# Performance work log

Hardware: AMD Instinct MI355X
Metric: run time of the kernel (lower is better)

## Reference

```python
import jax, jax.numpy as jnp
import numpy as np

# ---- static problem config (matches init_kwargs / input_specs) ----
L = 8                      # num_labels
D = H = W = 96             # volume dims
N = D * H * W
ALPHA, BETA, GAMMA = 8.0, 0.125, 3.0
NIT = 5                    # num_iterations
# 4-D bilateral grid dims: 3 spatial axes scaled by alpha, 1 intensity axis scaled by beta
GD = (int(np.ceil((D - 1) / ALPHA)) + 2,
      int(np.ceil((H - 1) / ALPHA)) + 2,
      int(np.ceil((W - 1) / ALPHA)) + 2,
      int(np.ceil(1.0 / BETA)) + 2)
GSIZE = int(np.prod(GD))
_STRIDES = np.array([GD[1] * GD[2] * GD[3], GD[2] * GD[3], GD[3], 1], dtype=np.int32)


def spatial_gaussian(Q):
    """Exact separable 3D Gaussian filter with sigma=GAMMA. Q: (L, D, H, W)."""
    r = int(3 * GAMMA)
    t = jnp.arange(-r, r + 1, dtype=Q.dtype)
    k = jnp.exp(-0.5 * (t / GAMMA) ** 2)
    k = k / k.sum()
    x = Q[None]  # (1, L, D, H, W)
    for ax in range(3):
        kspatial = [1, 1, 1]
        kspatial[ax] = 2 * r + 1
        kern = jnp.broadcast_to(k.reshape([1, 1] + kspatial), [L, 1] + kspatial)
        pad = [(r, r) if i == ax else (0, 0) for i in range(3)]
        x = jax.lax.conv_general_dilated(
            x, kern, (1, 1, 1), pad, feature_group_count=L,
            dimension_numbers=('NCDHW', 'OIDHW', 'NCDHW'))
    return x[0]


def splat_coords(img):
    """4-D lattice features per voxel. img: (D, H, W). Returns lo (4,N) int32, frac (4,N)."""
    zz, yy, xx = jnp.meshgrid(jnp.arange(D, dtype=img.dtype),
                              jnp.arange(H, dtype=img.dtype),
                              jnp.arange(W, dtype=img.dtype), indexing='ij')
    feats = jnp.stack([zz.reshape(-1) / ALPHA,
                       yy.reshape(-1) / ALPHA,
                       xx.reshape(-1) / ALPHA,
                       img.reshape(-1) / BETA], axis=0)  # (4, N)
    hi = jnp.asarray(GD, feats.dtype).reshape(4, 1) - 2.0
    lo_f = jnp.clip(jnp.floor(feats), 0.0, hi)
    frac = feats - lo_f
    return lo_f.astype(jnp.int32), frac


def blur1(g, ax):
    """[1,2,1]/4 blur along axis ax (grid-unit Gaussian of the splat-blur-slice)."""
    pad = [(0, 0)] * g.ndim
    pad[ax] = (1, 1)
    gp = jnp.pad(g, pad)
    n = g.shape[ax]
    a = jax.lax.slice_in_dim(gp, 0, n, axis=ax)
    b = jax.lax.slice_in_dim(gp, 1, n + 1, axis=ax)
    c = jax.lax.slice_in_dim(gp, 2, n + 2, axis=ax)
    return 0.25 * a + 0.5 * b + 0.25 * c


def lattice_filter(vals, lo, frac):
    """Splat-blur-slice high-dim Gaussian filter. vals: (C, N) -> (C, N)."""
    C = vals.shape[0]
    grid = jnp.zeros((C, GSIZE), vals.dtype)
    idxs, ws = [], []
    for bits in range(16):  # 16 corners of the 4-D cell (multilinear splat)
        off = np.array([(bits >> d) & 1 for d in range(4)], dtype=np.int32)
        w = jnp.prod(jnp.where(off[:, None] == 1, frac, 1.0 - frac), axis=0)  # (N,)
        idx = jnp.sum((lo + off[:, None]) * _STRIDES[:, None], axis=0)        # (N,)
        idxs.append(idx)
        ws.append(w)
        grid = grid.at[:, idx].add(vals * w[None])
    g = grid.reshape((C,) + GD)
    for ax in range(1, 5):
        g = blur1(g, ax)
    gf = g.reshape(C, GSIZE)
    out = jnp.zeros_like(vals)
    for bits in range(16):  # slice
        out = out + ws[bits][None] * gf[:, idxs[bits]]
    return out


def bilateral_apply(Q, lo, frac):
    """Normalized bilateral filtering of Q (L, D, H, W)."""
    vals = jnp.concatenate([Q.reshape(L, N), jnp.ones((1, N), Q.dtype)], axis=0)
    out = lattice_filter(vals, lo, frac)
    return (out[:L] / (out[L:] + 1e-8)).reshape(L, D, H, W)


def reference(U, image, spatial_ker_weights, bilateral_ker_weights, compatibility_matrix):
    Us = U[0]                               # (L, D, H, W); batch must be 1
    lo, frac = splat_coords(image[0, 0])    # lattice built once from image (as in __init__)
    Q = Us
    for _ in range(NIT):
        # NOTE: original code recomputes softmax of the (unchanged) unary U each iteration
        Qsm = jax.nn.softmax(Us, axis=0)
        sp = spatial_gaussian(Qsm).reshape(L, -1)
        bi = bilateral_apply(Qsm, lo, frac).reshape(L, -1)
        Qp = compatibility_matrix @ (spatial_ker_weights @ sp + bilateral_ker_weights @ bi)
        Q = Us + Qp.reshape(L, D, H, W)
    return jax.nn.softmax(Q, axis=0)[None]


def setup_inputs() -> dict:
    key = jax.random.key(0)
    k1, k2 = jax.random.split(key)
    U = jax.random.normal(k1, (1, L, D, H, W), jnp.float32)
    image = jax.random.uniform(k2, (1, 1, D, H, W), jnp.float32)
    eye = jnp.eye(L, dtype=jnp.float32)
    return {
        "U": U,
        "image": image,
        "spatial_ker_weights": 3.0 * eye,     # spatial_ker_weight * I
        "bilateral_ker_weights": 10.0 * eye,  # bilateral_ker_weight * I
        "compatibility_matrix": eye,
    }
```

## Files before the change

kernel.cpp:

```cpp
#include <hip/hip_runtime.h>
#include <math.h>

#define LBL   8
#define DIM   96
#define PLANE (DIM*DIM)
#define NVOX  (DIM*DIM*DIM)
#define GD0 14
#define GD1 14
#define GD2 14
#define GD3 10
#define GSIZE (GD0*GD1*GD2*GD3)
#define ST0 1960
#define ST1 140
#define ST2 10
#define CH  12
#define NBLK 12
#define NBLKS (NBLK*NBLK*NBLK)
#define PART 720
#define GOUT (GSIZE*9)
#define SUP 513
#define ROW8 (DIM/8)
#define PLANE8 (PLANE/8)
#define VOL8 (NVOX/8)

typedef _Float16 half8 __attribute__((ext_vector_type(8)));

__device__ inline half8 h8zero() {
    half8 v;
    #pragma unroll
    for (int e = 0; e < 8; ++e) v[e] = (_Float16)0.f;
    return v;
}

__constant__ float GW[10] = {
    0.13317604f, 0.12597912f, 0.10663904f, 0.08077540f, 0.05475300f,
    0.03320771f, 0.01802341f, 0.00875346f, 0.00380423f, 0.00147945f
};

__global__ __launch_bounds__(512)
void k_softmax_splat(const float* __restrict__ U, const float* __restrict__ img,
                     _Float16* __restrict__ q, float* __restrict__ part)
{
    __shared__ float sF[512];
    __shared__ __align__(16) unsigned char uball[2880 * 4];
    __shared__ _Float16 sA[64*180];

    _Float16* sU = (_Float16*)uball;
    float*    sB = (float*)uball;

    const int tid = threadIdx.x;
    const int bid0 = blockIdx.x;
    const int bid = (bid0 & 7) * (NBLKS >> 3) + (bid0 >> 3);
    const int bx = bid % NBLK;
    const int by = (bid / NBLK) % NBLK;
    const int bz = bid / (NBLK*NBLK);

    const int lx = tid & 7;
    const int ly = (tid >> 3) & 7;
    const int lz = tid >> 6;

    const int x = bx*8 + lx;
    const int y = by*8 + ly;
    const int z = bz*8 + lz;
    const int vox = z * PLANE + y * DIM + x;

    {
        float u[LBL];
        float m = -1e30f;
        #pragma unroll
        for (int l = 0; l < LBL; ++l) { u[l] = U[l*NVOX + vox]; m = fmaxf(m, u[l]); }
        float ssum = 0.f;
        #pragma unroll
        for (int l = 0; l < LBL; ++l) { u[l] = expf(u[l] - m); ssum += u[l]; }
        const float inv = 1.f / ssum;
        #pragma unroll
        for (int l = 0; l < LBL; ++l) {
            u[l] *= inv;
            q[l*NVOX + vox] = (_Float16)u[l];
            sU[l*SUP + tid] = (_Float16)u[l];
        }
        sU[8*SUP + tid] = (_Float16)1.0f;
        sF[tid] = img[vox] * 8.0f;
    }
    __syncthreads();

    {
        const int cgrp = tid & 3;
        const int k2   = (tid >> 2) & 1;
        const int row  = tid >> 3;
        const int cb   = cgrp * 2;

        float bins[10][3];
        #pragma unroll
        for (int g = 0; g < 10; ++g) { bins[g][0]=0.f; bins[g][1]=0.f; bins[g][2]=0.f; }

        for (int vx = 0; vx < 8; ++vx) {
            const int vi = row*8 + vx;
            const float f  = sF[vi];
            const float wx = k2 ? (float)vx*0.125f : 1.f - (float)vx*0.125f;
            const float u0 = (float)sU[cb*SUP + vi];
            const float u1 = (float)sU[(cb+1)*SUP + vi];
            const float u2 = (float)sU[8*SUP + vi];
            #pragma unroll
            for (int g = 0; g < 10; ++g) {
                float w = fmaxf(1.f - fabsf(f - (float)g), 0.f) * wx;
                bins[g][0] += w*u0; bins[g][1] += w*u1; bins[g][2] += w*u2;
            }
        }
        _Float16* pA = sA + row*180 + k2*90;
        #pragma unroll
        for (int g = 0; g < 10; ++g) {
            pA[g*9 + cb]     = (_Float16)bins[g][0];
            pA[g*9 + cb + 1] = (_Float16)bins[g][1];
            if (cgrp == 3) pA[g*9 + 8] = (_Float16)bins[g][2];
        }
    }
    __syncthreads();

    if (tid < 288) {
        const int c   = tid % 9;
        const int k2  = (tid / 9) & 1;
        const int j2  = (tid / 18) & 1;
        const int lzo = tid / 36;
        float S[10];
        #pragma unroll
        for (int g = 0; g < 10; ++g) S[g] = 0.f;
        for (int ly2 = 0; ly2 < 8; ++ly2) {
            const float wy = j2 ? (float)ly2*0.125f : 1.f - (float)ly2*0.125f;
            const _Float16* pA = sA + (lzo*8 + ly2)*180 + k2*90;
            #pragma unroll
            for (int g = 0; g < 10; ++g) S[g] += wy * (float)pA[g*9 + c];
        }
        float* pB = sB + lzo*360 + j2*180 + k2*90;
        #pragma unroll
        for (int g = 0; g < 10; ++g) pB[g*9 + c] = S[g];
    }
    __syncthreads();

    for (int item = tid; item < PART; item += 512) {
        const int t  = item / 90;
        const int gc = item % 90;
        const int i2 = t >> 2, j2 = (t >> 1) & 1, k2 = t & 1;
        float acc = 0.f;
        #pragma unroll
        for (int lzo = 0; lzo < 8; ++lzo) {
            const float wz = i2 ? (float)lzo*0.125f : 1.f - (float)lzo*0.125f;
            acc += wz * sB[lzo*360 + j2*180 + k2*90 + gc];
        }
        part[(size_t)bid*PART + item] = acc;
    }
}

__global__ __launch_bounds__(256)
void k_reduce(const float* __restrict__ part, float* __restrict__ grid)
{
    const int item = blockIdx.x*256 + threadIdx.x;
    if (item >= GOUT) return;
    const int c    = item % 9;
    const int cell = item / 9;
    const int gz = cell / ST0;
    int r = cell % ST0;
    const int gy = r / ST1;  r %= ST1;
    const int gx = r / ST2;
    const int g  = r % ST2;
    float acc = 0.f;
    #pragma unroll
    for (int t = 0; t < 8; ++t) {
        const int i2 = t >> 2, j2 = (t >> 1) & 1, k2 = t & 1;
        const int bz = gz - i2, by = gy - j2, bx = gx - k2;
        if ((unsigned)bz < (unsigned)NBLK && (unsigned)by < (unsigned)NBLK &&
            (unsigned)bx < (unsigned)NBLK)
            acc += part[(size_t)((bz*NBLK + by)*NBLK + bx)*PART + t*90 + g*9 + c];
    }
    grid[cell*CH + c] = acc;
}

__global__ __launch_bounds__(256)
void k_blur81(const float* __restrict__ src, float* __restrict__ dst)
{
    const int item = blockIdx.x*256 + threadIdx.x;
    if (item >= GOUT) return;
    const int c    = item % 9;
    const int cell = item / 9;
    const int gz = cell / ST0;
    int r = cell % ST0;
    const int gy = r / ST1;  r %= ST1;
    const int gx = r / ST2;
    const int g  = r % ST2;

    const int crd[4] = {gz, gy, gx, g};
    const int ext[4] = {GD0, GD1, GD2, GD3};
    const int str[4] = {ST0, ST1, ST2, 1};
    float wa[4][3];
    int   oa[4][3];
    #pragma unroll
    for (int ax = 0; ax < 4; ++ax)
        #pragma unroll
        for (int dd = 0; dd < 3; ++dd) {
            const int cc = crd[ax] + dd - 1;
            const bool ok = (cc >= 0 && cc < ext[ax]);
            wa[ax][dd] = ok ? (dd == 1 ? 0.5f : 0.25f) : 0.f;
            oa[ax][dd] = ok ? (dd - 1) * str[ax] : 0;
        }

    float acc = 0.f;
    #pragma unroll
    for (int a = 0; a < 3; ++a) {
        const float w0 = wa[0][a];
        #pragma unroll
        for (int b = 0; b < 3; ++b) {
            const float w1 = w0 * wa[1][b];
            #pragma unroll
            for (int d2 = 0; d2 < 3; ++d2) {
                const float w2 = w1 * wa[2][d2];
                const int ob = oa[0][a] + oa[1][b] + oa[2][d2];
                #pragma unroll
                for (int e = 0; e < 3; ++e)
                    acc += w2 * wa[3][e] * src[(cell + ob + oa[3][e])*CH + c];
            }
        }
    }
    dst[cell*CH + c] = acc;
}

__global__ __launch_bounds__(256)
void k_gauss_xy(const half8* __restrict__ src, half8* __restrict__ dst)
{
    __shared__ _Float16 sIn[PLANE];
    __shared__ _Float16 sX[PLANE];
    half8* sIn8 = (half8*)sIn;
    half8* sX8  = (half8*)sX;

    const int tid = threadIdx.x;
    const size_t base8 = (size_t)blockIdx.x * PLANE8;

    for (int i = tid; i < PLANE8; i += 256) sIn8[i] = src[base8 + i];
    __syncthreads();

    for (int it = tid; it < 576; it += 256) {
        const int seg = it % 6;
        const int row = it / 6;
        float w[48];
        #pragma unroll
        for (int k = 0; k < 6; ++k) {
            const int j8 = 2*seg - 2 + k;
            half8 v = h8zero();
            if (j8 >= 0 && j8 < ROW8) v = sIn8[row*ROW8 + j8];
            #pragma unroll
            for (int e = 0; e < 8; ++e) w[k*8 + e] = (float)v[e];
        }
        half8 o0 = h8zero(), o1 = h8zero();
        #pragma unroll
        for (int i = 0; i < 16; ++i) {
            float acc = 0.f;
            #pragma unroll
            for (int t = -9; t <= 9; ++t) acc += GW[t < 0 ? -t : t] * w[i + 16 + t];
            if (i < 8) o0[i] = (_Float16)acc; else o1[i - 8] = (_Float16)acc;
        }
        sX8[row*ROW8 + 2*seg]     = o0;
        sX8[row*ROW8 + 2*seg + 1] = o1;
    }
    __syncthreads();

    for (int it = tid; it < 288; it += 256) {
        const int x8   = it % ROW8;
        const int yseg = it / ROW8;
        const int ct = yseg * 4;
        float acc[4][8];
        #pragma unroll
        for (int k = 0; k < 4; ++k)
            #pragma unroll
            for (int e = 0; e < 8; ++e) acc[k][e] = 0.f;
        #pragma unroll
        for (int jj = 0; jj < 22; ++jj) {
            const int j = ct - 9 + jj;
            if (j < 0 || j >= DIM) continue;
            const half8 v = sX8[j*ROW8 + x8];
            float f[8];
            #pragma unroll
            for (int e = 0; e < 8; ++e) f[e] = (float)v[e];
            #pragma unroll
            for (int k = 0; k < 4; ++k) {
                const int d = jj - 9 - k;
                if (d >= -9 && d <= 9) {
                    const float wgt = GW[d < 0 ? -d : d];
                    #pragma unroll
                    for (int e = 0; e < 8; ++e) acc[k][e] += wgt * f[e];
                }
            }
        }
        #pragma unroll
        for (int k = 0; k < 4; ++k) {
            half8 o;
            #pragma unroll
            for (int e = 0; e < 8; ++e) o[e] = (_Float16)acc[k][e];
            dst[base8 + (ct + k)*ROW8 + x8] = o;
        }
    }
}

__global__ __launch_bounds__(256)
void k_gauss_z(const half8* __restrict__ src, half8* __restrict__ dst)
{
    const int bid = blockIdx.x;
    const int swz = (bid & 7) * (864 >> 3) + (bid >> 3);
    const int u = swz * 256 + threadIdx.x;

    const int x8 = u % ROW8;
    const int yy = (u / ROW8) % DIM;
    const int ztl = u / (ROW8 * DIM);
    const int zt = ztl % (DIM/4);
    const int l  = ztl / (DIM/4);
    const int base8 = l * VOL8 + yy * ROW8 + x8;
    const int ct = zt * 4;

    float acc[4][8];
    #pragma unroll
    for (int k = 0; k < 4; ++k)
        #pragma unroll
        for (int e = 0; e < 8; ++e) acc[k][e] = 0.f;

    #pragma unroll
    for (int jj = 0; jj < 22; ++jj) {
        const int j = ct - 9 + jj;
        if (j < 0 || j >= DIM) continue;
        const half8 v = src[base8 + j*PLANE8];
        float f[8];
        #pragma unroll
        for (int e = 0; e < 8; ++e) f[e] = (float)v[e];
        #pragma unroll
        for (int k = 0; k < 4; ++k) {
            const int d = jj - 9 - k;
            if (d >= -9 && d <= 9) {
                const float wgt = GW[d < 0 ? -d : d];
                #pragma unroll
                for (int e = 0; e < 8; ++e) acc[k][e] += wgt * f[e];
            }
        }
    }
    #pragma unroll
    for (int k = 0; k < 4; ++k) {
        half8 o;
        #pragma unroll
        for (int e = 0; e < 8; ++e) o[e] = (_Float16)acc[k][e];
        dst[base8 + (ct + k)*PLANE8] = o;
    }
}

__global__ __launch_bounds__(512)
void k_final(const float* __restrict__ U, const _Float16* __restrict__ sp,
             const float* __restrict__ grid, const float* __restrict__ img,
             const float* __restrict__ Cm, const float* __restrict__ Sw,
             const float* __restrict__ Bw, float* __restrict__ out)
{
    __shared__ float sm[128];
    __shared__ __align__(16) float sG[1800];

    const int tid = threadIdx.x;
    if (tid < 64) {
        const int i = tid >> 3, j = tid & 7;
        float cs = 0.f, cb = 0.f;
        #pragma unroll
        for (int k = 0; k < 8; ++k) {
            cs += Cm[i*8 + k] * Sw[k*8 + j];
            cb += Cm[i*8 + k] * Bw[k*8 + j];
        }
        sm[tid] = cs;
        sm[64 + tid] = cb;
    }

    const int bid0 = blockIdx.x;
    const int bid = (bid0 & 7) * (1728 >> 3) + (bid0 >> 3);
    const int bxi = bid % 3;
    const int byi = (bid / 3) % 6;
    const int z   = bid / 18;

    const int zc0 = z >> 3;
    const float fz = (float)(z & 7) * 0.125f;

    for (int item = tid; item < 1800; item += 512) {
        const int c    = item % 12;
        const int cell = item / 12;
        const int g  = cell % 10;
        const int xc = (cell / 10) % 5;
        const int yc = cell / 50;
        const int cellA = zc0*ST0 + (byi*2 + yc)*ST1 + (bxi*4 + xc)*ST2 + g;
        sG[item] = (1.f - fz)*grid[cellA*CH + c] + fz*grid[(cellA + ST0)*CH + c];
    }
    __syncthreads();

    const int lx  = tid & 31;
    const int lyt = tid >> 5;
    const int x = bxi*32 + lx;
    const int y = byi*16 + lyt;
    const int vox = z*PLANE + y*DIM + x;

    const float f = img[vox] * 8.0f;
    int li = (int)floorf(f);
    li = li < 0 ? 0 : (li > 8 ? 8 : li);
    const float fi = f - (float)li;
    const float fy = (float)(y & 7) * 0.125f;
    const float fx = (float)(x & 7) * 0.125f;
    const float wyv[2] = {1.f - fy, fy};
    const float wxv[2] = {1.f - fx, fx};
    const float wiv[2] = {1.f - fi, fi};
    const int ycb = lyt >> 3;
    const int xcb = lx >> 3;

    float acc[9];
    #pragma unroll
    for (int c = 0; c < 9; ++c) acc[c] = 0.f;

    #pragma unroll
    for (int j2 = 0; j2 < 2; ++j2)
    #pragma unroll
    for (int k2 = 0; k2 < 2; ++k2) {
        const float wsp = wyv[j2] * wxv[k2];
        const int base = (((ycb + j2)*5 + (xcb + k2))*10 + li)*12;
        #pragma unroll
        for (int m2 = 0; m2 < 2; ++m2) {
            const float w = wsp * wiv[m2];
            const float* p = &sG[base + m2*12];
            const float4 p0 = *reinterpret_cast<const float4*>(p);
            const float4 p1 = *reinterpret_cast<const float4*>(p + 4);
            acc[0] += w * p0.x; acc[1] += w * p0.y; acc[2] += w * p0.z; acc[3] += w * p0.w;
            acc[4] += w * p1.x; acc[5] += w * p1.y; acc[6] += w * p1.z; acc[7] += w * p1.w;
            acc[8] += w * p[8];
        }
    }
    const float dinv = 1.f / (acc[8] + 1e-8f);

    float spv[LBL], uu[LBL];
    #pragma unroll
    for (int l = 0; l < LBL; ++l) {
        spv[l] = (float)sp[(size_t)l*NVOX + vox];
        uu[l]  = U[(size_t)l*NVOX + vox];
    }

    float v[LBL];
    float mx = -1e30f;
    #pragma unroll
    for (int i = 0; i < LBL; ++i) {
        float t = 0.f;
        #pragma unroll
        for (int l = 0; l < LBL; ++l)
            t += sm[i*8 + l] * spv[l] + sm[64 + i*8 + l] * (acc[l] * dinv);
        v[i] = uu[i] + t;
        mx = fmaxf(mx, v[i]);
    }
    float ssum = 0.f;
    #pragma unroll
    for (int i = 0; i < LBL; ++i) { v[i] = expf(v[i] - mx); ssum += v[i]; }
    const float inv = 1.f / ssum;
    #pragma unroll
    for (int i = 0; i < LBL; ++i) out[i*NVOX + vox] = v[i] * inv;
}

extern "C" void kernel_launch(void* const* d_in, const int* in_sizes, int n_in,
                              void* d_out, int out_size, void* d_ws, size_t ws_size,
                              hipStream_t stream)
{
    const float* U   = (const float*)d_in[0];
    const float* img = (const float*)d_in[1];
    const float* Sw  = (const float*)d_in[2];
    const float* Bw  = (const float*)d_in[3];
    const float* Cm  = (const float*)d_in[4];
    float* out = (float*)d_out;

    _Float16* qh  = (_Float16*)d_ws;
    _Float16* g1h = qh + (size_t)LBL * NVOX;
    float* gridA  = (float*)(g1h + (size_t)LBL * NVOX);
    float* part   = gridA + (size_t)GSIZE * CH;
    float* gridB  = part;

    k_softmax_splat<<<NBLKS, 512, 0, stream>>>(U, img, qh, part);
    k_reduce<<<(GOUT + 255)/256, 256, 0, stream>>>(part, gridA);
    k_blur81<<<(GOUT + 255)/256, 256, 0, stream>>>(gridA, gridB);

    k_gauss_xy<<<768, 256, 0, stream>>>((const half8*)qh, (half8*)g1h);
    k_gauss_z<<<864, 256, 0, stream>>>((const half8*)g1h, (half8*)qh);

    k_final<<<1728, 512, 0, stream>>>(U, qh, gridB, img, Cm, Sw, Bw, out);
}
```

Baseline: 91.43 us.

## Splat via atomics into grid and fuse bilateral blur into xy Gaussian launch

Each splat block now atomically adds its partial sums straight into the lattice grid, which is zeroed by a memset. This replaces the separate partial buffer and reduce kernel. The 81-tap grid blur runs as extra blocks appended to the xy Gaussian launch, so the two independent stages share one kernel and two launches are removed. expf is also swapped for __expf in both softmaxes. In exchange the change adds atomic contention, makes float summation order nondeterministic, adds a memset, and uses the fast exp approximation.

```diff
diff --git a/kernel.cpp b/kernel.cpp
--- a/kernel.cpp
+++ b/kernel.cpp
@@ -22,6 +22,8 @@
 #define ROW8 (DIM/8)
 #define PLANE8 (PLANE/8)
 #define VOL8 (NVOX/8)
+#define XY_BLOCKS 768
+#define BLUR_BLOCKS ((GOUT + 255)/256)
 
 typedef _Float16 half8 __attribute__((ext_vector_type(8)));
 
@@ -39,7 +41,7 @@
 
 __global__ __launch_bounds__(512)
 void k_softmax_splat(const float* __restrict__ U, const float* __restrict__ img,
-                     _Float16* __restrict__ q, float* __restrict__ part)
+                     _Float16* __restrict__ q, float* __restrict__ grid)
 {
     __shared__ float sF[512];
     __shared__ __align__(16) unsigned char uball[2880 * 4];
@@ -71,7 +73,7 @@
         for (int l = 0; l < LBL; ++l) { u[l] = U[l*NVOX + vox]; m = fmaxf(m, u[l]); }
         float ssum = 0.f;
         #pragma unroll
-        for (int l = 0; l < LBL; ++l) { u[l] = expf(u[l] - m); ssum += u[l]; }
+        for (int l = 0; l < LBL; ++l) { u[l] = __expf(u[l] - m); ssum += u[l]; }
         const float inv = 1.f / ssum;
         #pragma unroll
         for (int l = 0; l < LBL; ++l) {
@@ -140,6 +142,8 @@
     for (int item = tid; item < PART; item += 512) {
         const int t  = item / 90;
         const int gc = item % 90;
+        const int g  = gc / 9;
+        const int c  = gc % 9;
         const int i2 = t >> 2, j2 = (t >> 1) & 1, k2 = t & 1;
         float acc = 0.f;
         #pragma unroll
@@ -147,91 +151,69 @@
             const float wz = i2 ? (float)lzo*0.125f : 1.f - (float)lzo*0.125f;
             acc += wz * sB[lzo*360 + j2*180 + k2*90 + gc];
         }
-        part[(size_t)bid*PART + item] = acc;
+        const int cell = (bz + i2)*ST0 + (by + j2)*ST1 + (bx + k2)*ST2 + g;
+        atomicAdd(&grid[cell*CH + c], acc);
     }
 }
 
 __global__ __launch_bounds__(256)
-void k_reduce(const float* __restrict__ part, float* __restrict__ grid)
-{
-    const int item = blockIdx.x*256 + threadIdx.x;
-    if (item >= GOUT) return;
-    const int c    = item % 9;
-    const int cell = item / 9;
-    const int gz = cell / ST0;
-    int r = cell % ST0;
-    const int gy = r / ST1;  r %= ST1;
-    const int gx = r / ST2;
-    const int g  = r % ST2;
-    float acc = 0.f;
-    #pragma unroll
-    for (int t = 0; t < 8; ++t) {
-        const int i2 = t >> 2, j2 = (t >> 1) & 1, k2 = t & 1;
-        const int bz = gz - i2, by = gy - j2, bx = gx - k2;
-        if ((unsigned)bz < (unsigned)NBLK && (unsigned)by < (unsigned)NBLK &&
-            (unsigned)bx < (unsigned)NBLK)
-            acc += part[(size_t)((bz*NBLK + by)*NBLK + bx)*PART + t*90 + g*9 + c];
-    }
-    grid[cell*CH + c] = acc;
-}
-
-__global__ __launch_bounds__(256)
-void k_blur81(const float* __restrict__ src, float* __restrict__ dst)
-{
-    const int item = blockIdx.x*256 + threadIdx.x;
-    if (item >= GOUT) return;
-    const int c    = item % 9;
-    const int cell = item / 9;
-    const int gz = cell / ST0;
-    int r = cell % ST0;
-    const int gy = r / ST1;  r %= ST1;
-    const int gx = r / ST2;
-    const int g  = r % ST2;
-
-    const int crd[4] = {gz, gy, gx, g};
-    const int ext[4] = {GD0, GD1, GD2, GD3};
-    const int str[4] = {ST0, ST1, ST2, 1};
-    float wa[4][3];
-    int   oa[4][3];
-    #pragma unroll
-    for (int ax = 0; ax < 4; ++ax)
-        #pragma unroll
-        for (int dd = 0; dd < 3; ++dd) {
-            const int cc = crd[ax] + dd - 1;
-            const bool ok = (cc >= 0 && cc < ext[ax]);
-            wa[ax][dd] = ok ? (dd == 1 ? 0.5f : 0.25f) : 0.f;
-            oa[ax][dd] = ok ? (dd - 1) * str[ax] : 0;
-        }
-
-    float acc = 0.f;
-    #pragma unroll
-    for (int a = 0; a < 3; ++a) {
-        const float w0 = wa[0][a];
-        #pragma unroll
-        for (int b = 0; b < 3; ++b) {
-            const float w1 = w0 * wa[1][b];
-            #pragma unroll
-            for (int d2 = 0; d2 < 3; ++d2) {
-                const float w2 = w1 * wa[2][d2];
-                const int ob = oa[0][a] + oa[1][b] + oa[2][d2];
-                #pragma unroll
-                for (int e = 0; e < 3; ++e)
-                    acc += w2 * wa[3][e] * src[(cell + ob + oa[3][e])*CH + c];
-            }
-        }
-    }
-    dst[cell*CH + c] = acc;
-}
-
-__global__ __launch_bounds__(256)
-void k_gauss_xy(const half8* __restrict__ src, half8* __restrict__ dst)
+void k_xy_blur(const half8* __restrict__ src, half8* __restrict__ dst,
+               const float* __restrict__ gsrc, float* __restrict__ gdst)
 {
     __shared__ _Float16 sIn[PLANE];
     __shared__ _Float16 sX[PLANE];
+
+    const int tid = threadIdx.x;
+
+    if (blockIdx.x >= XY_BLOCKS) {
+        const int item = (blockIdx.x - XY_BLOCKS)*256 + tid;
+        if (item >= GOUT) return;
+        const int c    = item % 9;
+        const int cell = item / 9;
+        const int gz = cell / ST0;
+        int r = cell % ST0;
+        const int gy = r / ST1;  r %= ST1;
+        const int gx = r / ST2;
+        const int g  = r % ST2;
+
+        const int crd[4] = {gz, gy, gx, g};
+        const int ext[4] = {GD0, GD1, GD2, GD3};
+        const int str[4] = {ST0, ST1, ST2, 1};
+        float wa[4][3];
+        int   oa[4][3];
+        #pragma unroll
+        for (int ax = 0; ax < 4; ++ax)
+            #pragma unroll
+            for (int dd = 0; dd < 3; ++dd) {
+                const int cc = crd[ax] + dd - 1;
+                const bool ok = (cc >= 0 && cc < ext[ax]);
+                wa[ax][dd] = ok ? (dd == 1 ? 0.5f : 0.25f) : 0.f;
+                oa[ax][dd] = ok ? (dd - 1) * str[ax] : 0;
+            }
+
+        float acc = 0.f;
+        #pragma unroll
+        for (int a = 0; a < 3; ++a) {
+            const float w0 = wa[0][a];
+            #pragma unroll
+            for (int b = 0; b < 3; ++b) {
+                const float w1 = w0 * wa[1][b];
+                #pragma unroll
+                for (int d2 = 0; d2 < 3; ++d2) {
+                    const float w2 = w1 * wa[2][d2];
+                    const int ob = oa[0][a] + oa[1][b] + oa[2][d2];
+                    #pragma unroll
+                    for (int e = 0; e < 3; ++e)
+                        acc += w2 * wa[3][e] * gsrc[(cell + ob + oa[3][e])*CH + c];
+                }
+            }
+        }
+        gdst[cell*CH + c] = acc;
+        return;
+    }
+
     half8* sIn8 = (half8*)sIn;
     half8* sX8  = (half8*)sX;
-
-    const int tid = threadIdx.x;
     const size_t base8 = (size_t)blockIdx.x * PLANE8;
 
     for (int i = tid; i < PLANE8; i += 256) sIn8[i] = src[base8 + i];
@@ -450,7 +432,7 @@
     }
     float ssum = 0.f;
     #pragma unroll
-    for (int i = 0; i < LBL; ++i) { v[i] = expf(v[i] - mx); ssum += v[i]; }
+    for (int i = 0; i < LBL; ++i) { v[i] = __expf(v[i] - mx); ssum += v[i]; }
     const float inv = 1.f / ssum;
     #pragma unroll
     for (int i = 0; i < LBL; ++i) out[i*NVOX + vox] = v[i] * inv;
@@ -470,14 +452,15 @@
     _Float16* qh  = (_Float16*)d_ws;
     _Float16* g1h = qh + (size_t)LBL * NVOX;
     float* gridA  = (float*)(g1h + (size_t)LBL * NVOX);
-    float* part   = gridA + (size_t)GSIZE * CH;
-    float* gridB  = part;
-
-    k_softmax_splat<<<NBLKS, 512, 0, stream>>>(U, img, qh, part);
-    k_reduce<<<(GOUT + 255)/256, 256, 0, stream>>>(part, gridA);
-    k_blur81<<<(GOUT + 255)/256, 256, 0, stream>>>(gridA, gridB);
-
-    k_gauss_xy<<<768, 256, 0, stream>>>((const half8*)qh, (half8*)g1h);
+    float* gridB  = gridA + (size_t)GSIZE * CH;
+
+    hipMemsetAsync(gridA, 0, (size_t)GSIZE * CH * sizeof(float), stream);
+
+    k_softmax_splat<<<NBLKS, 512, 0, stream>>>(U, img, qh, gridA);
+
+    k_xy_blur<<<XY_BLOCKS + BLUR_BLOCKS, 256, 0, stream>>>(
+        (const half8*)qh, (half8*)g1h, gridA, gridB);
+
     k_gauss_z<<<864, 256, 0, stream>>>((const half8*)g1h, (half8*)qh);
 
     k_final<<<1728, 512, 0, stream>>>(U, qh, gridB, img, Cm, Sw, Bw, out);
```

After: 78.67 us. 1.16x faster.
